# Kernel optimization log

Measured on AMD Instinct MI355X. Metric: run time of the kernel, lower is better.

Reference implementation:

```python
import jax, jax.numpy as jnp
import numpy as np

# Static network layout: inputs occupy columns [0, I), hidden [I, N-O), outputs [N-O, N)
B = 16384  # batch size
N = 1024   # total neurons
I = 128    # input neurons
O = 64     # output neurons
REFRACTORY = 0.9


def _activate(x, act_ids):
    """Vectorized per-neuron heterogeneous activation.
    act_ids: 0=relu, 1=tanh, 2=sigmoid, 3=identity.
    Replaces the original serial per-neuron getattr dispatch loop."""
    r = jax.nn.relu(x)
    t = jnp.tanh(x)
    s = jax.nn.sigmoid(x)
    return jnp.select([act_ids == 0, act_ids == 1, act_ids == 2], [r, t, s], x)


def setup_inputs() -> dict:
    key = jax.random.key(0)
    k0, k1, k2, k3, k4 = jax.random.split(key, 5)
    return {
        "prev_states": jax.random.normal(k0, (B, N), jnp.float32),
        "input_values": jax.random.normal(k1, (B, I), jnp.float32),
        "weight_matrix": jax.random.normal(k2, (N, N), jnp.float32) * 0.05,
        "biases": jax.random.normal(k3, (N,), jnp.float32) * 0.1,
        "act_ids": jax.random.randint(k4, (N,), 0, 4, dtype=jnp.int32),
    }


def reference(prev_states, input_values, weight_matrix, biases, act_ids):
    # _apply_refractory_factor on hidden cols + _assign_input_values on input cols
    states = jnp.concatenate(
        [input_values,
         prev_states[:, I:N - O] * REFRACTORY,
         prev_states[:, N - O:]],
        axis=1)  # [B, N]
    # total_input = states @ W + b
    total = states @ weight_matrix + biases  # [B, N]
    # activation applied to every non-input neuron; input neurons keep their state
    activated = _activate(total, act_ids[None, :])  # [B, N]
    new_states = jnp.concatenate([states[:, :I], activated[:, I:]], axis=1)
    # return output-layer slice
    return new_states[:, N - O:]
```

## Files before the change

kernel.cpp:

```cpp
#include <hip/hip_runtime.h>
#include <math.h>

#define BATCH 16384
#define NN    1024
#define NI    128
#define NO    64
#define REFR  0.9f

typedef float  f32x4  __attribute__((ext_vector_type(4)));
typedef __bf16 bf16x8 __attribute__((ext_vector_type(8)));

__global__ __launch_bounds__(256) void pack_w_kernel(const float* __restrict__ W,
                                                     __bf16* __restrict__ wsB) {
    int idx = blockIdx.x * 256 + threadIdx.x;
    int k = idx >> 6;
    int n = idx & 63;
    float v = W[(size_t)k * NN + (NN - NO) + n];
    int kc = k >> 5;
    if (kc >= 4 && kc < 30) v *= REFR;
    int kk = k & 31;
    int r3 = kk >> 3;
    int j  = kk & 7;
    int tn = n >> 4;
    int l  = r3 * 16 + (n & 15);
    wsB[(size_t)(((kc * 4 + tn) * 64 + l) * 8 + j)] = (__bf16)v;
}

__device__ inline float activate(float x, int id) {
    if (id == 0) return fmaxf(x, 0.0f);
    if (id == 1) return tanhf(x);
    if (id == 2) return 1.0f / (1.0f + __expf(-x));
    return x;
}

__global__ __launch_bounds__(256, 2) void fused_rnn_kernel(
    const float* __restrict__ prev,
    const float* __restrict__ inp,
    const __bf16* __restrict__ wsB,
    const float* __restrict__ bias,
    const int*  __restrict__ act,
    float* __restrict__ out)
{
    const int lane = threadIdx.x & 63;
    const int wv   = threadIdx.x >> 6;
    const int m    = lane & 15;
    const int q    = lane >> 4;
    const int row0 = blockIdx.x * 32;

    const float* prow0 = prev + (size_t)(row0 + m) * NN;
    const float* prow1 = prev + (size_t)(row0 + 16 + m) * NN;
    const float* irow0 = inp  + (size_t)(row0 + m) * NI;
    const float* irow1 = inp  + (size_t)(row0 + 16 + m) * NI;
    const bf16x8* Bf   = (const bf16x8*)wsB;
    const int qo = q * 8;

    f32x4 acc0[4], acc1[4];
#pragma unroll
    for (int t = 0; t < 4; ++t) {
        acc0[t] = (f32x4){0.f, 0.f, 0.f, 0.f};
        acc1[t] = acc0[t];
    }

    f32x4 A0a[8], A0b[8], A1a[8], A1b[8];

#define LOADC(i) {                                                           \
        const int kc_ = wv * 8 + (i);                                        \
        const float* s0_ = (kc_ < 4) ? irow0 : prow0;                        \
        const float* s1_ = (kc_ < 4) ? irow1 : prow1;                        \
        const f32x4* p0_ = (const f32x4*)(s0_ + kc_ * 32 + qo);              \
        const f32x4* p1_ = (const f32x4*)(s1_ + kc_ * 32 + qo);              \
        A0a[i] = __builtin_nontemporal_load(p0_);                            \
        A0b[i] = __builtin_nontemporal_load(p0_ + 1);                        \
        A1a[i] = __builtin_nontemporal_load(p1_);                            \
        A1b[i] = __builtin_nontemporal_load(p1_ + 1);                        \
    }

#pragma unroll
    for (int i = 0; i < 4; ++i) LOADC(i)

#pragma unroll
    for (int i = 0; i < 8; ++i) {
        if (i < 4) LOADC(i + 4)
        const int kc = wv * 8 + i;

        bf16x8 a0, a1;
#pragma unroll
        for (int e = 0; e < 4; ++e) {
            a0[e]     = (__bf16)A0a[i][e];
            a0[e + 4] = (__bf16)A0b[i][e];
            a1[e]     = (__bf16)A1a[i][e];
            a1[e + 4] = (__bf16)A1b[i][e];
        }

        const bf16x8* bp = Bf + (size_t)kc * 256 + lane;
        bf16x8 b0 = bp[0];
        bf16x8 b1 = bp[64];
        bf16x8 b2 = bp[128];
        bf16x8 b3 = bp[192];

        acc0[0] = __builtin_amdgcn_mfma_f32_16x16x32_bf16(a0, b0, acc0[0], 0, 0, 0);
        acc1[0] = __builtin_amdgcn_mfma_f32_16x16x32_bf16(a1, b0, acc1[0], 0, 0, 0);
        acc0[1] = __builtin_amdgcn_mfma_f32_16x16x32_bf16(a0, b1, acc0[1], 0, 0, 0);
        acc1[1] = __builtin_amdgcn_mfma_f32_16x16x32_bf16(a1, b1, acc1[1], 0, 0, 0);
        acc0[2] = __builtin_amdgcn_mfma_f32_16x16x32_bf16(a0, b2, acc0[2], 0, 0, 0);
        acc1[2] = __builtin_amdgcn_mfma_f32_16x16x32_bf16(a1, b2, acc1[2], 0, 0, 0);
        acc0[3] = __builtin_amdgcn_mfma_f32_16x16x32_bf16(a0, b3, acc0[3], 0, 0, 0);
        acc1[3] = __builtin_amdgcn_mfma_f32_16x16x32_bf16(a1, b3, acc1[3], 0, 0, 0);
    }
#undef LOADC

    __shared__ __align__(16) float red[4][2][16][68];
#pragma unroll
    for (int t = 0; t < 4; ++t) {
#pragma unroll
        for (int r = 0; r < 4; ++r) {
            red[wv][0][q * 4 + r][t * 16 + m] = acc0[t][r];
            red[wv][1][q * 4 + r][t * 16 + m] = acc1[t][r];
        }
    }
    __syncthreads();

    const int orow = threadIdx.x >> 4;
    const int oc   = (threadIdx.x & 15) * 4;

    f32x4 s0 = *(const f32x4*)&red[0][0][orow][oc];
    f32x4 s1 = *(const f32x4*)&red[0][1][orow][oc];
#pragma unroll
    for (int w = 1; w < 4; ++w) {
        s0 += *(const f32x4*)&red[w][0][orow][oc];
        s1 += *(const f32x4*)&red[w][1][orow][oc];
    }

    const float* bo = bias + (NN - NO);
    const int*   ao = act  + (NN - NO);
    f32x4 o0, o1;
#pragma unroll
    for (int c = 0; c < 4; ++c) {
        const float b  = bo[oc + c];
        const int   id = ao[oc + c];
        o0[c] = activate(s0[c] + b, id);
        o1[c] = activate(s1[c] + b, id);
    }
    *(f32x4*)(out + (size_t)(row0 + orow) * NO + oc)      = o0;
    *(f32x4*)(out + (size_t)(row0 + 16 + orow) * NO + oc) = o1;
}

extern "C" void kernel_launch(void* const* d_in, const int* in_sizes, int n_in,
                              void* d_out, int out_size, void* d_ws, size_t ws_size,
                              hipStream_t stream) {
    const float* prev = (const float*)d_in[0];
    const float* inp  = (const float*)d_in[1];
    const float* W    = (const float*)d_in[2];
    const float* bias = (const float*)d_in[3];
    const int*   act  = (const int*)  d_in[4];
    float* out = (float*)d_out;
    __bf16* wsB = (__bf16*)d_ws;

    pack_w_kernel<<<256, 256, 0, stream>>>(W, wsB);

    fused_rnn_kernel<<<BATCH / 32, 256, 0, stream>>>(prev, inp, wsB, bias, act, out);
}
```

Measured before the change: 118.0 us.

## Fuse weight packing into main kernel via per-block LDS staging

Removes the separate weight-pack kernel launch. Each 512-thread block now converts the 1024x64 output-column weight slice to bf16, applies the refractory scale and stores it in 128KB of LDS. It then runs the MFMA loop on 64 rows, with two row halves split across 8 waves, before reducing and activating. This saves a launch and the global round trip for packed weights. In exchange, every block re-reads and converts W with strided scalar loads, and the large LDS footprint limits occupancy to one block per CU.

```diff
diff --git a/kernel.cpp b/kernel.cpp
--- a/kernel.cpp
+++ b/kernel.cpp
@@ -10,22 +10,6 @@
 typedef float  f32x4  __attribute__((ext_vector_type(4)));
 typedef __bf16 bf16x8 __attribute__((ext_vector_type(8)));
 
-__global__ __launch_bounds__(256) void pack_w_kernel(const float* __restrict__ W,
-                                                     __bf16* __restrict__ wsB) {
-    int idx = blockIdx.x * 256 + threadIdx.x;
-    int k = idx >> 6;
-    int n = idx & 63;
-    float v = W[(size_t)k * NN + (NN - NO) + n];
-    int kc = k >> 5;
-    if (kc >= 4 && kc < 30) v *= REFR;
-    int kk = k & 31;
-    int r3 = kk >> 3;
-    int j  = kk & 7;
-    int tn = n >> 4;
-    int l  = r3 * 16 + (n & 15);
-    wsB[(size_t)(((kc * 4 + tn) * 64 + l) * 8 + j)] = (__bf16)v;
-}
-
 __device__ inline float activate(float x, int id) {
     if (id == 0) return fmaxf(x, 0.0f);
     if (id == 1) return tanhf(x);
@@ -33,38 +17,37 @@
     return x;
 }
 
-__global__ __launch_bounds__(256, 2) void fused_rnn_kernel(
+__global__ __launch_bounds__(512, 1) void fused_rnn_kernel(
     const float* __restrict__ prev,
     const float* __restrict__ inp,
-    const __bf16* __restrict__ wsB,
+    const float* __restrict__ W,
     const float* __restrict__ bias,
     const int*  __restrict__ act,
     float* __restrict__ out)
 {
-    const int lane = threadIdx.x & 63;
-    const int wv   = threadIdx.x >> 6;
+    __shared__ __align__(16) char smem[131072];
+    __bf16* wlds = (__bf16*)smem;
+    float*  redf = (float*)smem;
+
+    const int tid  = threadIdx.x;
+    const int lane = tid & 63;
+    const int wv   = tid >> 6;
+    const int ks   = wv & 3;
+    const int mh   = wv >> 2;
     const int m    = lane & 15;
     const int q    = lane >> 4;
-    const int row0 = blockIdx.x * 32;
+    const int qo   = q * 8;
+    const int row0 = blockIdx.x * 64;
 
-    const float* prow0 = prev + (size_t)(row0 + m) * NN;
-    const float* prow1 = prev + (size_t)(row0 + 16 + m) * NN;
-    const float* irow0 = inp  + (size_t)(row0 + m) * NI;
-    const float* irow1 = inp  + (size_t)(row0 + 16 + m) * NI;
-    const bf16x8* Bf   = (const bf16x8*)wsB;
-    const int qo = q * 8;
-
-    f32x4 acc0[4], acc1[4];
-#pragma unroll
-    for (int t = 0; t < 4; ++t) {
-        acc0[t] = (f32x4){0.f, 0.f, 0.f, 0.f};
-        acc1[t] = acc0[t];
-    }
+    const float* prow0 = prev + (size_t)(row0 + mh * 32 + m) * NN;
+    const float* prow1 = prev + (size_t)(row0 + mh * 32 + 16 + m) * NN;
+    const float* irow0 = inp  + (size_t)(row0 + mh * 32 + m) * NI;
+    const float* irow1 = inp  + (size_t)(row0 + mh * 32 + 16 + m) * NI;
 
     f32x4 A0a[8], A0b[8], A1a[8], A1b[8];
 
 #define LOADC(i) {                                                           \
-        const int kc_ = wv * 8 + (i);                                        \
+        const int kc_ = ks * 8 + (i);                                        \
         const float* s0_ = (kc_ < 4) ? irow0 : prow0;                        \
         const float* s1_ = (kc_ < 4) ? irow1 : prow1;                        \
         const f32x4* p0_ = (const f32x4*)(s0_ + kc_ * 32 + qo);              \
@@ -78,10 +61,35 @@
 #pragma unroll
     for (int i = 0; i < 4; ++i) LOADC(i)
 
+    for (int it = 0; it < 16; ++it) {
+        const int f  = it * 512 + tid;
+        const int kc = f >> 8;
+        const int tn = (f >> 6) & 3;
+        const int l  = f & 63;
+        const int col  = (NN - NO) + tn * 16 + (l & 15);
+        const int rowb = kc * 32 + ((l >> 4) << 3);
+        const float sc = (kc >= 4 && kc < 30) ? REFR : 1.0f;
+        bf16x8 frag;
+#pragma unroll
+        for (int j = 0; j < 8; ++j) {
+            float v = W[(size_t)(rowb + j) * NN + col] * sc;
+            frag[j] = (__bf16)v;
+        }
+        *(bf16x8*)(wlds + (size_t)f * 8) = frag;
+    }
+    __syncthreads();
+
+    f32x4 acc0[4], acc1[4];
+#pragma unroll
+    for (int t = 0; t < 4; ++t) {
+        acc0[t] = (f32x4){0.f, 0.f, 0.f, 0.f};
+        acc1[t] = acc0[t];
+    }
+
 #pragma unroll
     for (int i = 0; i < 8; ++i) {
         if (i < 4) LOADC(i + 4)
-        const int kc = wv * 8 + i;
+        const int kc = ks * 8 + i;
 
         bf16x8 a0, a1;
 #pragma unroll
@@ -92,7 +100,7 @@
             a1[e + 4] = (__bf16)A1b[i][e];
         }
 
-        const bf16x8* bp = Bf + (size_t)kc * 256 + lane;
+        const bf16x8* bp = (const bf16x8*)wlds + (size_t)kc * 256 + lane;
         bf16x8 b0 = bp[0];
         bf16x8 b1 = bp[64];
         bf16x8 b2 = bp[128];
@@ -109,40 +117,42 @@
     }
 #undef LOADC
 
-    __shared__ __align__(16) float red[4][2][16][68];
+    __syncthreads();
+
 #pragma unroll
     for (int t = 0; t < 4; ++t) {
 #pragma unroll
         for (int r = 0; r < 4; ++r) {
-            red[wv][0][q * 4 + r][t * 16 + m] = acc0[t][r];
-            red[wv][1][q * 4 + r][t * 16 + m] = acc1[t][r];
+            redf[((((mh * 4 + ks) * 2 + 0) * 16 + (q * 4 + r)) * 68) + t * 16 + m] = acc0[t][r];
+            redf[((((mh * 4 + ks) * 2 + 1) * 16 + (q * 4 + r)) * 68) + t * 16 + m] = acc1[t][r];
         }
     }
     __syncthreads();
 
-    const int orow = threadIdx.x >> 4;
-    const int oc   = (threadIdx.x & 15) * 4;
-
-    f32x4 s0 = *(const f32x4*)&red[0][0][orow][oc];
-    f32x4 s1 = *(const f32x4*)&red[0][1][orow][oc];
-#pragma unroll
-    for (int w = 1; w < 4; ++w) {
-        s0 += *(const f32x4*)&red[w][0][orow][oc];
-        s1 += *(const f32x4*)&red[w][1][orow][oc];
-    }
-
     const float* bo = bias + (NN - NO);
     const int*   ao = act  + (NN - NO);
-    f32x4 o0, o1;
 #pragma unroll
-    for (int c = 0; c < 4; ++c) {
-        const float b  = bo[oc + c];
-        const int   id = ao[oc + c];
-        o0[c] = activate(s0[c] + b, id);
-        o1[c] = activate(s1[c] + b, id);
+    for (int pass = 0; pass < 2; ++pass) {
+        const int T  = pass * 512 + tid;
+        const int r  = T >> 4;
+        const int oc = (T & 15) * 4;
+        const int rmh = r >> 5;
+        const int rtl = (r >> 4) & 1;
+        const int rm  = r & 15;
+
+        f32x4 s = *(const f32x4*)&redf[((((rmh * 4 + 0) * 2 + rtl) * 16 + rm) * 68) + oc];
+#pragma unroll
+        for (int k = 1; k < 4; ++k) {
+            s += *(const f32x4*)&redf[((((rmh * 4 + k) * 2 + rtl) * 16 + rm) * 68) + oc];
+        }
+
+        f32x4 o;
+#pragma unroll
+        for (int c = 0; c < 4; ++c) {
+            o[c] = activate(s[c] + bo[oc + c], ao[oc + c]);
+        }
+        *(f32x4*)(out + (size_t)(row0 + r) * NO + oc) = o;
     }
-    *(f32x4*)(out + (size_t)(row0 + orow) * NO + oc)      = o0;
-    *(f32x4*)(out + (size_t)(row0 + 16 + orow) * NO + oc) = o1;
 }
 
 extern "C" void kernel_launch(void* const* d_in, const int* in_sizes, int n_in,
@@ -154,9 +164,7 @@
     const float* bias = (const float*)d_in[3];
     const int*   act  = (const int*)  d_in[4];
     float* out = (float*)d_out;
-    __bf16* wsB = (__bf16*)d_ws;
+    (void)d_ws; (void)ws_size;
 
-    pack_w_kernel<<<256, 256, 0, stream>>>(W, wsB);
-
-    fused_rnn_kernel<<<BATCH / 32, 256, 0, stream>>>(prev, inp, wsB, bias, act, out);
+    fused_rnn_kernel<<<BATCH / 64, 512, 0, stream>>>(prev, inp, W, bias, act, out);
 }
```

After: 117.4 us. Within noise of the previous version (-0.5%).
